# Optimization experiments

Hardware: AMD Instinct MI355X
Metric: run time of the kernel (lower is better)

## Reference

```python
import jax, jax.numpy as jnp
import numpy as np

N = 50000
E = 800000
IN_CH = 256
HID = 32
HEADS = 4
OUT_CH = 40
NEG_SLOPE = 0.2
BN_EPS = 1e-5


def _gat_conv(x, W, att_src, att_dst, bias, src, dst, num_nodes, concat):
    # x: [N, F_in]; W: [F_in, H*C]; att_src/att_dst: [H, C]
    H, C = att_src.shape
    h = (x @ W).reshape(num_nodes, H, C)            # [N, H, C]
    a_src = (h * att_src[None]).sum(-1)             # [N, H]
    a_dst = (h * att_dst[None]).sum(-1)             # [N, H]
    e = jax.nn.leaky_relu(a_src[src] + a_dst[dst], NEG_SLOPE)  # [Etot, H]
    # segment softmax over incoming edges of each destination node
    m = jax.ops.segment_max(e, dst, num_segments=num_nodes)    # [N, H]
    ex = jnp.exp(e - m[dst])
    s = jax.ops.segment_sum(ex, dst, num_segments=num_nodes)   # [N, H]
    alpha = ex / (s[dst] + 1e-16)                   # [Etot, H]
    out = jax.ops.segment_sum(h[src] * alpha[:, :, None], dst,
                              num_segments=num_nodes)          # [N, H, C]
    out = out.reshape(num_nodes, H * C) if concat else out.mean(axis=1)
    return out + bias


def setup_inputs() -> dict:
    key = jax.random.key(0)
    ks = jax.random.split(key, 12)
    x = jax.random.normal(ks[0], (N, IN_CH), dtype=jnp.float32)
    edge_index = jax.random.randint(ks[1], (2, E), 0, N, dtype=jnp.int64)
    # layer 1: in -> heads*hid, concat
    W1 = jax.random.normal(ks[2], (IN_CH, HEADS * HID), dtype=jnp.float32) * (1.0 / np.sqrt(IN_CH))
    att_src1 = jax.random.normal(ks[3], (HEADS, HID), dtype=jnp.float32) * 0.1
    att_dst1 = jax.random.normal(ks[4], (HEADS, HID), dtype=jnp.float32) * 0.1
    b1 = jnp.zeros((HEADS * HID,), dtype=jnp.float32)
    # batch norm over hidden*heads features
    gamma = jnp.ones((HEADS * HID,), dtype=jnp.float32)
    beta = jnp.zeros((HEADS * HID,), dtype=jnp.float32)
    # layer 2: heads*hid -> out, heads=1, mean (concat=False)
    W2 = jax.random.normal(ks[5], (HEADS * HID, OUT_CH), dtype=jnp.float32) * (1.0 / np.sqrt(HEADS * HID))
    att_src2 = jax.random.normal(ks[6], (1, OUT_CH), dtype=jnp.float32) * 0.1
    att_dst2 = jax.random.normal(ks[7], (1, OUT_CH), dtype=jnp.float32) * 0.1
    b2 = jnp.zeros((OUT_CH,), dtype=jnp.float32)
    return {"x": x, "edge_index": edge_index, "W1": W1, "att_src1": att_src1,
            "att_dst1": att_dst1, "b1": b1, "gamma": gamma, "beta": beta,
            "W2": W2, "att_src2": att_src2, "att_dst2": att_dst2, "b2": b2}


def reference(x, edge_index, W1, att_src1, att_dst1, b1, gamma, beta,
              W2, att_src2, att_dst2, b2):
    num_nodes = x.shape[0]
    loops = jnp.arange(num_nodes, dtype=edge_index.dtype)
    src = jnp.concatenate([edge_index[0], loops])   # add self-loops (PyG default)
    dst = jnp.concatenate([edge_index[1], loops])
    h = _gat_conv(x, W1, att_src1, att_dst1, b1, src, dst, num_nodes, concat=True)
    # BatchNorm over nodes (training-mode batch statistics)
    mu = h.mean(axis=0)
    var = h.var(axis=0)
    h = (h - mu) * jax.lax.rsqrt(var + BN_EPS) * gamma + beta
    h = jax.nn.elu(h)
    out = _gat_conv(h, W2, att_src2, att_dst2, b2, src, dst, num_nodes, concat=False)
    return out
```

## Files before the change

kernel.cpp:

```cpp
#include <hip/hip_runtime.h>

#define NN 50000
#define EE 800000
#define FIN 256
#define F1 128
#define F2 40
#define CAP 48
#define G1B ((NN + 127) / 128)
#define FILLB ((EE + 255) / 256)
#define PB ((NN + 63) / 64)

typedef unsigned int u32;
typedef unsigned short u16;

static __device__ __forceinline__ u32 f2bf(float f) {
  u32 u = __float_as_uint(f);
  return (u + 0x7FFFu + ((u >> 16) & 1u)) >> 16;
}
#define BF_LO(u) __uint_as_float((u) << 16)
#define BF_HI(u) __uint_as_float((u) & 0xFFFF0000u)

__global__ __launch_bounds__(256) void g1f_kernel(const float* __restrict__ x,
                                                  const float* __restrict__ W1,
                                                  const float* __restrict__ att_src,
                                                  const float* __restrict__ att_dst,
                                                  u32* __restrict__ h1bf,
                                                  float* __restrict__ a_src,
                                                  float* __restrict__ a_dst,
                                                  const int* __restrict__ ei,
                                                  int* __restrict__ cnt,
                                                  int* __restrict__ csr) {
  __shared__ float Alds[16 * 132];
  __shared__ float Blds[16 * 128];
  __shared__ float att_s[128], att_d[128];
  const int t = threadIdx.x;

  if (blockIdx.x >= G1B) {
    int e = (blockIdx.x - G1B) * 256 + t;
    if (e < EE) {
      int src = ei[e];
      int dst = ei[EE + e];
      int p = atomicAdd(cnt + dst, 1);
      if (p < CAP) csr[dst * CAP + p] = src;
    }
    return;
  }

  if (t < 128) { att_s[t] = att_src[t]; att_d[t] = att_dst[t]; }
  const int m0 = blockIdx.x * 128;
  const int arow = t >> 1;
  const int akk = (t & 1) * 8;
  const int brow = t >> 4;
  const int bc = (t & 15) * 8;
  const int ty = t >> 4;
  const int tx = t & 15;

  float acc[8][8];
#pragma unroll
  for (int i = 0; i < 8; ++i)
#pragma unroll
    for (int j = 0; j < 8; ++j) acc[i][j] = 0.f;

  for (int k0 = 0; k0 < FIN; k0 += 16) {
    float4 a0 = {0.f, 0.f, 0.f, 0.f}, a1 = {0.f, 0.f, 0.f, 0.f};
    int gr = m0 + arow;
    if (gr < NN) {
      a0 = *(const float4*)(x + (size_t)gr * FIN + k0 + akk);
      a1 = *(const float4*)(x + (size_t)gr * FIN + k0 + akk + 4);
    }
    float4 b0 = *(const float4*)(W1 + (size_t)(k0 + brow) * F1 + bc);
    float4 b1 = *(const float4*)(W1 + (size_t)(k0 + brow) * F1 + bc + 4);
    __syncthreads();
    Alds[(akk + 0) * 132 + arow] = a0.x;
    Alds[(akk + 1) * 132 + arow] = a0.y;
    Alds[(akk + 2) * 132 + arow] = a0.z;
    Alds[(akk + 3) * 132 + arow] = a0.w;
    Alds[(akk + 4) * 132 + arow] = a1.x;
    Alds[(akk + 5) * 132 + arow] = a1.y;
    Alds[(akk + 6) * 132 + arow] = a1.z;
    Alds[(akk + 7) * 132 + arow] = a1.w;
    *(float4*)(Blds + brow * 128 + bc) = b0;
    *(float4*)(Blds + brow * 128 + bc + 4) = b1;
    __syncthreads();
#pragma unroll
    for (int k = 0; k < 16; ++k) {
      float4 av0 = *(const float4*)(Alds + k * 132 + ty * 8);
      float4 av1 = *(const float4*)(Alds + k * 132 + ty * 8 + 4);
      float4 bv0 = *(const float4*)(Blds + k * 128 + tx * 8);
      float4 bv1 = *(const float4*)(Blds + k * 128 + tx * 8 + 4);
      float aa[8] = {av0.x, av0.y, av0.z, av0.w, av1.x, av1.y, av1.z, av1.w};
      float bb[8] = {bv0.x, bv0.y, bv0.z, bv0.w, bv1.x, bv1.y, bv1.z, bv1.w};
#pragma unroll
      for (int i = 0; i < 8; ++i)
#pragma unroll
        for (int j = 0; j < 8; ++j) acc[i][j] = fmaf(aa[i], bb[j], acc[i][j]);
    }
  }
#pragma unroll
  for (int i = 0; i < 8; ++i) {
    int gr = m0 + ty * 8 + i;
    if (gr < NN) {
      uint4 w;
      w.x = f2bf(acc[i][0]) | (f2bf(acc[i][1]) << 16);
      w.y = f2bf(acc[i][2]) | (f2bf(acc[i][3]) << 16);
      w.z = f2bf(acc[i][4]) | (f2bf(acc[i][5]) << 16);
      w.w = f2bf(acc[i][6]) | (f2bf(acc[i][7]) << 16);
      *(uint4*)(h1bf + ((size_t)(tx >> 2) * NN + gr) * 16 + (tx & 3) * 4) = w;
    }
  }
#pragma unroll
  for (int i = 0; i < 8; ++i) {
    float ps = 0.f, pd = 0.f;
#pragma unroll
    for (int j = 0; j < 8; ++j) {
      int c = tx * 8 + j;
      ps += acc[i][j] * att_s[c];
      pd += acc[i][j] * att_d[c];
    }
    ps += __shfl_xor(ps, 1); pd += __shfl_xor(pd, 1);
    ps += __shfl_xor(ps, 2); pd += __shfl_xor(pd, 2);
    if ((tx & 3) == 0) {
      int gr = m0 + ty * 8 + i;
      if (gr < NN) {
        int head = tx >> 2;
        a_src[gr * 4 + head] = ps;
        a_dst[gr * 4 + head] = pd;
      }
    }
  }
}

__global__ __launch_bounds__(256) void gather1_kernel(const int* __restrict__ cnt,
                                                      const int* __restrict__ csr,
                                                      const float* __restrict__ a_src,
                                                      const float* __restrict__ a_dst,
                                                      const u32* __restrict__ h1bf,
                                                      const float* __restrict__ b1,
                                                      float* __restrict__ h1b,
                                                      float* __restrict__ bnsum,
                                                      float* __restrict__ bnsq) {
  __shared__ float bns[32], bnq[32];
  int t = threadIdx.x;
  if (t < 32) { bns[t] = 0.f; bnq[t] = 0.f; }
  __syncthreads();
  int d = blockIdx.x;
  int xcd = d & 7;
  int p = xcd >> 1;
  int nb = ((d >> 3) << 1) + (xcd & 1);
  int n = nb * 64 + (t >> 2);
  int l = t & 3;
  int f0 = p * 32 + l * 8;
  if (n < NN) {
    float adst = a_dst[n * 4 + p];
    float acc[8] = {0.f, 0.f, 0.f, 0.f, 0.f, 0.f, 0.f, 0.f};
    float ssum = 0.f;
    const u32* hb = h1bf + (size_t)p * NN * 16 + l * 4;
    {
      float e0 = a_src[n * 4 + p] + adst;
      e0 = e0 > 0.f ? e0 : 0.2f * e0;
      float x0 = __expf(e0);
      uint4 q = *(const uint4*)(hb + (size_t)n * 16);
      acc[0] = fmaf(x0, BF_LO(q.x), acc[0]); acc[1] = fmaf(x0, BF_HI(q.x), acc[1]);
      acc[2] = fmaf(x0, BF_LO(q.y), acc[2]); acc[3] = fmaf(x0, BF_HI(q.y), acc[3]);
      acc[4] = fmaf(x0, BF_LO(q.z), acc[4]); acc[5] = fmaf(x0, BF_HI(q.z), acc[5]);
      acc[6] = fmaf(x0, BF_LO(q.w), acc[6]); acc[7] = fmaf(x0, BF_HI(q.w), acc[7]);
      ssum += x0;
    }
    const int* row = csr + n * CAP;
    int m = cnt[n]; if (m > CAP) m = CAP;
    int i = 0;
    for (; i + 3 < m; i += 4) {
      int4 s4 = *(const int4*)(row + i);
      float e0 = a_src[s4.x * 4 + p] + adst;
      float e1 = a_src[s4.y * 4 + p] + adst;
      float e2 = a_src[s4.z * 4 + p] + adst;
      float e3 = a_src[s4.w * 4 + p] + adst;
      uint4 q0 = *(const uint4*)(hb + (size_t)s4.x * 16);
      uint4 q1 = *(const uint4*)(hb + (size_t)s4.y * 16);
      uint4 q2 = *(const uint4*)(hb + (size_t)s4.z * 16);
      uint4 q3 = *(const uint4*)(hb + (size_t)s4.w * 16);
      e0 = e0 > 0.f ? e0 : 0.2f * e0;  float x0 = __expf(e0);
      e1 = e1 > 0.f ? e1 : 0.2f * e1;  float x1 = __expf(e1);
      e2 = e2 > 0.f ? e2 : 0.2f * e2;  float x2 = __expf(e2);
      e3 = e3 > 0.f ? e3 : 0.2f * e3;  float x3 = __expf(e3);
      acc[0] = fmaf(x0, BF_LO(q0.x), acc[0]); acc[1] = fmaf(x0, BF_HI(q0.x), acc[1]);
      acc[2] = fmaf(x0, BF_LO(q0.y), acc[2]); acc[3] = fmaf(x0, BF_HI(q0.y), acc[3]);
      acc[4] = fmaf(x0, BF_LO(q0.z), acc[4]); acc[5] = fmaf(x0, BF_HI(q0.z), acc[5]);
      acc[6] = fmaf(x0, BF_LO(q0.w), acc[6]); acc[7] = fmaf(x0, BF_HI(q0.w), acc[7]);
      acc[0] = fmaf(x1, BF_LO(q1.x), acc[0]); acc[1] = fmaf(x1, BF_HI(q1.x), acc[1]);
      acc[2] = fmaf(x1, BF_LO(q1.y), acc[2]); acc[3] = fmaf(x1, BF_HI(q1.y), acc[3]);
      acc[4] = fmaf(x1, BF_LO(q1.z), acc[4]); acc[5] = fmaf(x1, BF_HI(q1.z), acc[5]);
      acc[6] = fmaf(x1, BF_LO(q1.w), acc[6]); acc[7] = fmaf(x1, BF_HI(q1.w), acc[7]);
      acc[0] = fmaf(x2, BF_LO(q2.x), acc[0]); acc[1] = fmaf(x2, BF_HI(q2.x), acc[1]);
      acc[2] = fmaf(x2, BF_LO(q2.y), acc[2]); acc[3] = fmaf(x2, BF_HI(q2.y), acc[3]);
      acc[4] = fmaf(x2, BF_LO(q2.z), acc[4]); acc[5] = fmaf(x2, BF_HI(q2.z), acc[5]);
      acc[6] = fmaf(x2, BF_LO(q2.w), acc[6]); acc[7] = fmaf(x2, BF_HI(q2.w), acc[7]);
      acc[0] = fmaf(x3, BF_LO(q3.x), acc[0]); acc[1] = fmaf(x3, BF_HI(q3.x), acc[1]);
      acc[2] = fmaf(x3, BF_LO(q3.y), acc[2]); acc[3] = fmaf(x3, BF_HI(q3.y), acc[3]);
      acc[4] = fmaf(x3, BF_LO(q3.z), acc[4]); acc[5] = fmaf(x3, BF_HI(q3.z), acc[5]);
      acc[6] = fmaf(x3, BF_LO(q3.w), acc[6]); acc[7] = fmaf(x3, BF_HI(q3.w), acc[7]);
      ssum += x0 + x1 + x2 + x3;
    }
    for (; i < m; ++i) {
      int s0 = row[i];
      float e0 = a_src[s0 * 4 + p] + adst;
      e0 = e0 > 0.f ? e0 : 0.2f * e0;
      float x0 = __expf(e0);
      uint4 q = *(const uint4*)(hb + (size_t)s0 * 16);
      acc[0] = fmaf(x0, BF_LO(q.x), acc[0]); acc[1] = fmaf(x0, BF_HI(q.x), acc[1]);
      acc[2] = fmaf(x0, BF_LO(q.y), acc[2]); acc[3] = fmaf(x0, BF_HI(q.y), acc[3]);
      acc[4] = fmaf(x0, BF_LO(q.z), acc[4]); acc[5] = fmaf(x0, BF_HI(q.z), acc[5]);
      acc[6] = fmaf(x0, BF_LO(q.w), acc[6]); acc[7] = fmaf(x0, BF_HI(q.w), acc[7]);
      ssum += x0;
    }
    float inv = 1.f / (ssum + 1e-16f);
    float4 b0 = *(const float4*)(b1 + f0);
    float4 b4 = *(const float4*)(b1 + f0 + 4);
    float o[8];
    o[0] = acc[0] * inv + b0.x; o[1] = acc[1] * inv + b0.y;
    o[2] = acc[2] * inv + b0.z; o[3] = acc[3] * inv + b0.w;
    o[4] = acc[4] * inv + b4.x; o[5] = acc[5] * inv + b4.y;
    o[6] = acc[6] * inv + b4.z; o[7] = acc[7] * inv + b4.w;
    float4 w0 = {o[0], o[1], o[2], o[3]};
    float4 w1 = {o[4], o[5], o[6], o[7]};
    *(float4*)(h1b + (size_t)n * F1 + f0) = w0;
    *(float4*)(h1b + (size_t)n * F1 + f0 + 4) = w1;
    int lb = l * 8;
#pragma unroll
    for (int j = 0; j < 8; ++j) {
      atomicAdd(&bns[lb + j], o[j]);
      atomicAdd(&bnq[lb + j], o[j] * o[j]);
    }
  }
  __syncthreads();
  if (t < 32) {
    atomicAdd(bnsum + p * 32 + t, bns[t]);
    atomicAdd(bnsq + p * 32 + t, bnq[t]);
  }
}

__global__ __launch_bounds__(256) void gemm2_kernel(const float* __restrict__ hpre,
                                                    const float* __restrict__ W2,
                                                    const float* __restrict__ bnsum,
                                                    const float* __restrict__ bnsq,
                                                    const float* __restrict__ gamma,
                                                    const float* __restrict__ beta,
                                                    u16* __restrict__ h2a,
                                                    u16* __restrict__ h2b,
                                                    const float* __restrict__ att_src2,
                                                    const float* __restrict__ att_dst2,
                                                    float* __restrict__ a_src2,
                                                    float* __restrict__ a_dst2) {
  __shared__ float Wlds[128 * 40];
  __shared__ float Alds[16 * 128];
  __shared__ float sc[128], sh[128];
  int t = threadIdx.x;
  for (int i = t; i < 128 * 40; i += 256) Wlds[i] = W2[i];
  if (t < 128) {
    const float invN = 1.f / (float)NN;
    float mu = bnsum[t] * invN;
    float var = bnsq[t] * invN - mu * mu;
    float s = gamma[t] * rsqrtf(var + 1e-5f);
    sc[t] = s;
    sh[t] = beta[t] - mu * s;
  }
  int tr = t >> 3;
  int tc = t & 7;
  float as5[5], ad5[5];
#pragma unroll
  for (int j = 0; j < 5; ++j) { as5[j] = att_src2[tc * 5 + j]; ad5[j] = att_dst2[tc * 5 + j]; }
  int n0 = blockIdx.x * 128;
  int lrow = t >> 1;
  int lkk = (t & 1) * 8;
  float acc[4][5];
#pragma unroll
  for (int i = 0; i < 4; ++i)
#pragma unroll
    for (int j = 0; j < 5; ++j) acc[i][j] = 0.f;

  for (int k0 = 0; k0 < F1; k0 += 16) {
    float av[8];
    int gn = n0 + lrow;
    if (gn < NN) {
      float4 v0 = *(const float4*)(hpre + (size_t)gn * F1 + k0 + lkk);
      float4 v1 = *(const float4*)(hpre + (size_t)gn * F1 + k0 + lkk + 4);
      av[0] = v0.x; av[1] = v0.y; av[2] = v0.z; av[3] = v0.w;
      av[4] = v1.x; av[5] = v1.y; av[6] = v1.z; av[7] = v1.w;
    } else {
#pragma unroll
      for (int j = 0; j < 8; ++j) av[j] = 0.f;
    }
    __syncthreads();
#pragma unroll
    for (int j = 0; j < 8; ++j) {
      int kg = k0 + lkk + j;
      float a = av[j] * sc[kg] + sh[kg];
      a = a > 0.f ? a : (__expf(a) - 1.f);
      Alds[(lkk + j) * 128 + lrow] = a;
    }
    __syncthreads();
#pragma unroll
    for (int k = 0; k < 16; ++k) {
      float4 a4 = *(const float4*)(Alds + k * 128 + tr * 4);
      float aa[4] = {a4.x, a4.y, a4.z, a4.w};
      float w[5];
#pragma unroll
      for (int j = 0; j < 5; ++j) w[j] = Wlds[(k0 + k) * 40 + tc * 5 + j];
#pragma unroll
      for (int i = 0; i < 4; ++i)
#pragma unroll
        for (int j = 0; j < 5; ++j) acc[i][j] = fmaf(aa[i], w[j], acc[i][j]);
    }
  }
#pragma unroll
  for (int i = 0; i < 4; ++i) {
    int gn = n0 + tr * 4 + i;
    if (gn < NN) {
#pragma unroll
      for (int j = 0; j < 5; ++j) {
        int f = tc * 5 + j;
        u16 v = (u16)f2bf(acc[i][j]);
        if (f < 32) h2a[(size_t)gn * 32 + f] = v;
        else        h2b[(size_t)gn * 8 + (f - 32)] = v;
      }
    }
  }
#pragma unroll
  for (int i = 0; i < 4; ++i) {
    float ps = 0.f, pd = 0.f;
#pragma unroll
    for (int j = 0; j < 5; ++j) { ps += acc[i][j] * as5[j]; pd += acc[i][j] * ad5[j]; }
#pragma unroll
    for (int off = 1; off < 8; off <<= 1) {
      ps += __shfl_xor(ps, off);
      pd += __shfl_xor(pd, off);
    }
    if (tc == 0) {
      int gn = n0 + tr * 4 + i;
      if (gn < NN) { a_src2[gn] = ps; a_dst2[gn] = pd; }
    }
  }
}

__global__ __launch_bounds__(256) void gather2_kernel(const int* __restrict__ cnt,
                                                      const int* __restrict__ csr,
                                                      const float* __restrict__ a_src,
                                                      const float* __restrict__ a_dst,
                                                      const u32* __restrict__ h2a,
                                                      const u32* __restrict__ h2b,
                                                      const float* __restrict__ b2,
                                                      float* __restrict__ out) {
  int t = threadIdx.x;
  int n = blockIdx.x * 32 + (t >> 3);
  if (n >= NN) return;
  int l = t & 7;
  bool act = (l < 5);
  bool isA = (l < 4);
  float adst = a_dst[n];
  float acc[8] = {0.f, 0.f, 0.f, 0.f, 0.f, 0.f, 0.f, 0.f};
  float ssum = 0.f;
  const uint4 zz = {0u, 0u, 0u, 0u};
  {
    float e0 = a_src[n] + adst;
    e0 = e0 > 0.f ? e0 : 0.2f * e0;
    float x0 = __expf(e0);
    uint4 q = act ? (isA ? *(const uint4*)(h2a + (size_t)n * 16 + l * 4)
                         : *(const uint4*)(h2b + (size_t)n * 4)) : zz;
    acc[0] = fmaf(x0, BF_LO(q.x), acc[0]); acc[1] = fmaf(x0, BF_HI(q.x), acc[1]);
    acc[2] = fmaf(x0, BF_LO(q.y), acc[2]); acc[3] = fmaf(x0, BF_HI(q.y), acc[3]);
    acc[4] = fmaf(x0, BF_LO(q.z), acc[4]); acc[5] = fmaf(x0, BF_HI(q.z), acc[5]);
    acc[6] = fmaf(x0, BF_LO(q.w), acc[6]); acc[7] = fmaf(x0, BF_HI(q.w), acc[7]);
    ssum += x0;
  }
  const int* row = csr + n * CAP;
  int m = cnt[n]; if (m > CAP) m = CAP;
  int i = 0;
  for (; i + 3 < m; i += 4) {
    int4 s4 = *(const int4*)(row + i);
    float e0 = a_src[s4.x] + adst;
    float e1 = a_src[s4.y] + adst;
    float e2 = a_src[s4.z] + adst;
    float e3 = a_src[s4.w] + adst;
    uint4 q0 = act ? (isA ? *(const uint4*)(h2a + (size_t)s4.x * 16 + l * 4)
                          : *(const uint4*)(h2b + (size_t)s4.x * 4)) : zz;
    uint4 q1 = act ? (isA ? *(const uint4*)(h2a + (size_t)s4.y * 16 + l * 4)
                          : *(const uint4*)(h2b + (size_t)s4.y * 4)) : zz;
    uint4 q2 = act ? (isA ? *(const uint4*)(h2a + (size_t)s4.z * 16 + l * 4)
                          : *(const uint4*)(h2b + (size_t)s4.z * 4)) : zz;
    uint4 q3 = act ? (isA ? *(const uint4*)(h2a + (size_t)s4.w * 16 + l * 4)
                          : *(const uint4*)(h2b + (size_t)s4.w * 4)) : zz;
    e0 = e0 > 0.f ? e0 : 0.2f * e0;  float x0 = __expf(e0);
    e1 = e1 > 0.f ? e1 : 0.2f * e1;  float x1 = __expf(e1);
    e2 = e2 > 0.f ? e2 : 0.2f * e2;  float x2 = __expf(e2);
    e3 = e3 > 0.f ? e3 : 0.2f * e3;  float x3 = __expf(e3);
    acc[0] = fmaf(x0, BF_LO(q0.x), acc[0]); acc[1] = fmaf(x0, BF_HI(q0.x), acc[1]);
    acc[2] = fmaf(x0, BF_LO(q0.y), acc[2]); acc[3] = fmaf(x0, BF_HI(q0.y), acc[3]);
    acc[4] = fmaf(x0, BF_LO(q0.z), acc[4]); acc[5] = fmaf(x0, BF_HI(q0.z), acc[5]);
    acc[6] = fmaf(x0, BF_LO(q0.w), acc[6]); acc[7] = fmaf(x0, BF_HI(q0.w), acc[7]);
    acc[0] = fmaf(x1, BF_LO(q1.x), acc[0]); acc[1] = fmaf(x1, BF_HI(q1.x), acc[1]);
    acc[2] = fmaf(x1, BF_LO(q1.y), acc[2]); acc[3] = fmaf(x1, BF_HI(q1.y), acc[3]);
    acc[4] = fmaf(x1, BF_LO(q1.z), acc[4]); acc[5] = fmaf(x1, BF_HI(q1.z), acc[5]);
    acc[6] = fmaf(x1, BF_LO(q1.w), acc[6]); acc[7] = fmaf(x1, BF_HI(q1.w), acc[7]);
    acc[0] = fmaf(x2, BF_LO(q2.x), acc[0]); acc[1] = fmaf(x2, BF_HI(q2.x), acc[1]);
    acc[2] = fmaf(x2, BF_LO(q2.y), acc[2]); acc[3] = fmaf(x2, BF_HI(q2.y), acc[3]);
    acc[4] = fmaf(x2, BF_LO(q2.z), acc[4]); acc[5] = fmaf(x2, BF_HI(q2.z), acc[5]);
    acc[6] = fmaf(x2, BF_LO(q2.w), acc[6]); acc[7] = fmaf(x2, BF_HI(q2.w), acc[7]);
    acc[0] = fmaf(x3, BF_LO(q3.x), acc[0]); acc[1] = fmaf(x3, BF_HI(q3.x), acc[1]);
    acc[2] = fmaf(x3, BF_LO(q3.y), acc[2]); acc[3] = fmaf(x3, BF_HI(q3.y), acc[3]);
    acc[4] = fmaf(x3, BF_LO(q3.z), acc[4]); acc[5] = fmaf(x3, BF_HI(q3.z), acc[5]);
    acc[6] = fmaf(x3, BF_LO(q3.w), acc[6]); acc[7] = fmaf(x3, BF_HI(q3.w), acc[7]);
    ssum += x0 + x1 + x2 + x3;
  }
  for (; i < m; ++i) {
    int s0 = row[i];
    float e0 = a_src[s0] + adst;
    e0 = e0 > 0.f ? e0 : 0.2f * e0;
    float x0 = __expf(e0);
    uint4 q = act ? (isA ? *(const uint4*)(h2a + (size_t)s0 * 16 + l * 4)
                         : *(const uint4*)(h2b + (size_t)s0 * 4)) : zz;
    acc[0] = fmaf(x0, BF_LO(q.x), acc[0]); acc[1] = fmaf(x0, BF_HI(q.x), acc[1]);
    acc[2] = fmaf(x0, BF_LO(q.y), acc[2]); acc[3] = fmaf(x0, BF_HI(q.y), acc[3]);
    acc[4] = fmaf(x0, BF_LO(q.z), acc[4]); acc[5] = fmaf(x0, BF_HI(q.z), acc[5]);
    acc[6] = fmaf(x0, BF_LO(q.w), acc[6]); acc[7] = fmaf(x0, BF_HI(q.w), acc[7]);
    ssum += x0;
  }
  float inv = 1.f / (ssum + 1e-16f);
  if (act) {
    float* op = out + (size_t)n * F2 + l * 8;
#pragma unroll
    for (int j = 0; j < 8; ++j) op[j] = acc[j] * inv + b2[l * 8 + j];
  }
}

extern "C" void kernel_launch(void* const* d_in, const int* in_sizes, int n_in,
                              void* d_out, int out_size, void* d_ws, size_t ws_size,
                              hipStream_t stream) {
  const float* x        = (const float*)d_in[0];
  const int*   ei       = (const int*)d_in[1];
  const float* W1       = (const float*)d_in[2];
  const float* att_src1 = (const float*)d_in[3];
  const float* att_dst1 = (const float*)d_in[4];
  const float* b1       = (const float*)d_in[5];
  const float* gamma    = (const float*)d_in[6];
  const float* beta     = (const float*)d_in[7];
  const float* W2       = (const float*)d_in[8];
  const float* att_src2 = (const float*)d_in[9];
  const float* att_dst2 = (const float*)d_in[10];
  const float* b2       = (const float*)d_in[11];
  float* out = (float*)d_out;

  int* cnt      = (int*)d_ws;
  float* bnsum  = (float*)(cnt + 50048);
  float* bnsq   = bnsum + 128;
  int* csr      = (int*)(bnsq + 128);
  u32* h1bf     = (u32*)(csr + NN * CAP);
  float* h1b    = (float*)(h1bf + 3200000);
  u32* h2a      = (u32*)(h1b + 6400000);
  u32* h2b      = h2a + 800000;
  float* a_src1 = (float*)(h2b + 200000);
  float* a_dst1 = a_src1 + 200000;
  float* a_src2 = a_dst1 + 200000;
  float* a_dst2 = a_src2 + 50000;

  hipMemsetAsync(cnt, 0, (50048 + 256) * sizeof(int), stream);

  g1f_kernel<<<G1B + FILLB, 256, 0, stream>>>(x, W1, att_src1, att_dst1,
                                              h1bf, a_src1, a_dst1,
                                              ei, cnt, csr);
  gather1_kernel<<<4 * PB, 256, 0, stream>>>(cnt, csr, a_src1, a_dst1,
                                             h1bf, b1, h1b, bnsum, bnsq);
  gemm2_kernel<<<(NN + 127) / 128, 256, 0, stream>>>(h1b, W2, bnsum, bnsq,
                                                     gamma, beta,
                                                     (u16*)h2a, (u16*)h2b,
                                                     att_src2, att_dst2,
                                                     a_src2, a_dst2);
  gather2_kernel<<<(NN + 31) / 32, 256, 0, stream>>>(cnt, csr, a_src2, a_dst2,
                                                     h2a, h2b, b2, out);
}
```

Before: 318.5 us.

## Split each node's edge list across more lanes in both gather kernels

```diff
diff --git a/kernel.cpp b/kernel.cpp
--- a/kernel.cpp
+++ b/kernel.cpp
@@ -8,7 +8,8 @@
 #define CAP 48
 #define G1B ((NN + 127) / 128)
 #define FILLB ((EE + 255) / 256)
-#define PB ((NN + 63) / 64)
+#define G1PB 3126
+#define G2B ((NN + 15) / 16)
 
 typedef unsigned int u32;
 typedef unsigned short u16;
@@ -147,15 +148,17 @@
   int xcd = d & 7;
   int p = xcd >> 1;
   int nb = ((d >> 3) << 1) + (xcd & 1);
-  int n = nb * 64 + (t >> 2);
-  int l = t & 3;
+  int n = nb * 16 + (t >> 4);
+  int sub = t & 15;
+  int g = sub >> 2;
+  int l = sub & 3;
   int f0 = p * 32 + l * 8;
+  float acc[8] = {0.f, 0.f, 0.f, 0.f, 0.f, 0.f, 0.f, 0.f};
+  float ssum = 0.f;
   if (n < NN) {
     float adst = a_dst[n * 4 + p];
-    float acc[8] = {0.f, 0.f, 0.f, 0.f, 0.f, 0.f, 0.f, 0.f};
-    float ssum = 0.f;
     const u32* hb = h1bf + (size_t)p * NN * 16 + l * 4;
-    {
+    if (g == 0) {
       float e0 = a_src[n * 4 + p] + adst;
       e0 = e0 > 0.f ? e0 : 0.2f * e0;
       float x0 = __expf(e0);
@@ -168,21 +171,16 @@
     }
     const int* row = csr + n * CAP;
     int m = cnt[n]; if (m > CAP) m = CAP;
-    int i = 0;
-    for (; i + 3 < m; i += 4) {
-      int4 s4 = *(const int4*)(row + i);
-      float e0 = a_src[s4.x * 4 + p] + adst;
-      float e1 = a_src[s4.y * 4 + p] + adst;
-      float e2 = a_src[s4.z * 4 + p] + adst;
-      float e3 = a_src[s4.w * 4 + p] + adst;
-      uint4 q0 = *(const uint4*)(hb + (size_t)s4.x * 16);
-      uint4 q1 = *(const uint4*)(hb + (size_t)s4.y * 16);
-      uint4 q2 = *(const uint4*)(hb + (size_t)s4.z * 16);
-      uint4 q3 = *(const uint4*)(hb + (size_t)s4.w * 16);
+    int i = g;
+    for (; i + 4 < m; i += 8) {
+      int s0 = row[i];
+      int s1 = row[i + 4];
+      float e0 = a_src[s0 * 4 + p] + adst;
+      float e1 = a_src[s1 * 4 + p] + adst;
+      uint4 q0 = *(const uint4*)(hb + (size_t)s0 * 16);
+      uint4 q1 = *(const uint4*)(hb + (size_t)s1 * 16);
       e0 = e0 > 0.f ? e0 : 0.2f * e0;  float x0 = __expf(e0);
       e1 = e1 > 0.f ? e1 : 0.2f * e1;  float x1 = __expf(e1);
-      e2 = e2 > 0.f ? e2 : 0.2f * e2;  float x2 = __expf(e2);
-      e3 = e3 > 0.f ? e3 : 0.2f * e3;  float x3 = __expf(e3);
       acc[0] = fmaf(x0, BF_LO(q0.x), acc[0]); acc[1] = fmaf(x0, BF_HI(q0.x), acc[1]);
       acc[2] = fmaf(x0, BF_LO(q0.y), acc[2]); acc[3] = fmaf(x0, BF_HI(q0.y), acc[3]);
       acc[4] = fmaf(x0, BF_LO(q0.z), acc[4]); acc[5] = fmaf(x0, BF_HI(q0.z), acc[5]);
@@ -191,17 +189,9 @@
       acc[2] = fmaf(x1, BF_LO(q1.y), acc[2]); acc[3] = fmaf(x1, BF_HI(q1.y), acc[3]);
       acc[4] = fmaf(x1, BF_LO(q1.z), acc[4]); acc[5] = fmaf(x1, BF_HI(q1.z), acc[5]);
       acc[6] = fmaf(x1, BF_LO(q1.w), acc[6]); acc[7] = fmaf(x1, BF_HI(q1.w), acc[7]);
-      acc[0] = fmaf(x2, BF_LO(q2.x), acc[0]); acc[1] = fmaf(x2, BF_HI(q2.x), acc[1]);
-      acc[2] = fmaf(x2, BF_LO(q2.y), acc[2]); acc[3] = fmaf(x2, BF_HI(q2.y), acc[3]);
-      acc[4] = fmaf(x2, BF_LO(q2.z), acc[4]); acc[5] = fmaf(x2, BF_HI(q2.z), acc[5]);
-      acc[6] = fmaf(x2, BF_LO(q2.w), acc[6]); acc[7] = fmaf(x2, BF_HI(q2.w), acc[7]);
-      acc[0] = fmaf(x3, BF_LO(q3.x), acc[0]); acc[1] = fmaf(x3, BF_HI(q3.x), acc[1]);
-      acc[2] = fmaf(x3, BF_LO(q3.y), acc[2]); acc[3] = fmaf(x3, BF_HI(q3.y), acc[3]);
-      acc[4] = fmaf(x3, BF_LO(q3.z), acc[4]); acc[5] = fmaf(x3, BF_HI(q3.z), acc[5]);
-      acc[6] = fmaf(x3, BF_LO(q3.w), acc[6]); acc[7] = fmaf(x3, BF_HI(q3.w), acc[7]);
-      ssum += x0 + x1 + x2 + x3;
-    }
-    for (; i < m; ++i) {
+      ssum += x0 + x1;
+    }
+    for (; i < m; i += 4) {
       int s0 = row[i];
       float e0 = a_src[s0 * 4 + p] + adst;
       e0 = e0 > 0.f ? e0 : 0.2f * e0;
@@ -213,6 +203,15 @@
       acc[6] = fmaf(x0, BF_LO(q.w), acc[6]); acc[7] = fmaf(x0, BF_HI(q.w), acc[7]);
       ssum += x0;
     }
+  }
+#pragma unroll
+  for (int j = 0; j < 8; ++j) {
+    acc[j] += __shfl_xor(acc[j], 4);
+    acc[j] += __shfl_xor(acc[j], 8);
+  }
+  ssum += __shfl_xor(ssum, 4);
+  ssum += __shfl_xor(ssum, 8);
+  if (n < NN && g == 0) {
     float inv = 1.f / (ssum + 1e-16f);
     float4 b0 = *(const float4*)(b1 + f0);
     float4 b4 = *(const float4*)(b1 + f0 + 4);
@@ -351,16 +350,17 @@
                                                       const float* __restrict__ b2,
                                                       float* __restrict__ out) {
   int t = threadIdx.x;
-  int n = blockIdx.x * 32 + (t >> 3);
+  int n = blockIdx.x * 16 + (t >> 4);
   if (n >= NN) return;
   int l = t & 7;
+  int g = (t >> 3) & 1;
   bool act = (l < 5);
   bool isA = (l < 4);
   float adst = a_dst[n];
   float acc[8] = {0.f, 0.f, 0.f, 0.f, 0.f, 0.f, 0.f, 0.f};
   float ssum = 0.f;
   const uint4 zz = {0u, 0u, 0u, 0u};
-  {
+  if (g == 0) {
     float e0 = a_src[n] + adst;
     e0 = e0 > 0.f ? e0 : 0.2f * e0;
     float x0 = __expf(e0);
@@ -374,58 +374,63 @@
   }
   const int* row = csr + n * CAP;
   int m = cnt[n]; if (m > CAP) m = CAP;
-  int i = 0;
-  for (; i + 3 < m; i += 4) {
-    int4 s4 = *(const int4*)(row + i);
-    float e0 = a_src[s4.x] + adst;
-    float e1 = a_src[s4.y] + adst;
-    float e2 = a_src[s4.z] + adst;
-    float e3 = a_src[s4.w] + adst;
-    uint4 q0 = act ? (isA ? *(const uint4*)(h2a + (size_t)s4.x * 16 + l * 4)
-                          : *(const uint4*)(h2b + (size_t)s4.x * 4)) : zz;
-    uint4 q1 = act ? (isA ? *(const uint4*)(h2a + (size_t)s4.y * 16 + l * 4)
-                          : *(const uint4*)(h2b + (size_t)s4.y * 4)) : zz;
-    uint4 q2 = act ? (isA ? *(const uint4*)(h2a + (size_t)s4.z * 16 + l * 4)
-                          : *(const uint4*)(h2b + (size_t)s4.z * 4)) : zz;
-    uint4 q3 = act ? (isA ? *(const uint4*)(h2a + (size_t)s4.w * 16 + l * 4)
-                          : *(const uint4*)(h2b + (size_t)s4.w * 4)) : zz;
-    e0 = e0 > 0.f ? e0 : 0.2f * e0;  float x0 = __expf(e0);
-    e1 = e1 > 0.f ? e1 : 0.2f * e1;  float x1 = __expf(e1);
-    e2 = e2 > 0.f ? e2 : 0.2f * e2;  float x2 = __expf(e2);
-    e3 = e3 > 0.f ? e3 : 0.2f * e3;  float x3 = __expf(e3);
-    acc[0] = fmaf(x0, BF_LO(q0.x), acc[0]); acc[1] = fmaf(x0, BF_HI(q0.x), acc[1]);
-    acc[2] = fmaf(x0, BF_LO(q0.y), acc[2]); acc[3] = fmaf(x0, BF_HI(q0.y), acc[3]);
-    acc[4] = fmaf(x0, BF_LO(q0.z), acc[4]); acc[5] = fmaf(x0, BF_HI(q0.z), acc[5]);
-    acc[6] = fmaf(x0, BF_LO(q0.w), acc[6]); acc[7] = fmaf(x0, BF_HI(q0.w), acc[7]);
-    acc[0] = fmaf(x1, BF_LO(q1.x), acc[0]); acc[1] = fmaf(x1, BF_HI(q1.x), acc[1]);
-    acc[2] = fmaf(x1, BF_LO(q1.y), acc[2]); acc[3] = fmaf(x1, BF_HI(q1.y), acc[3]);
-    acc[4] = fmaf(x1, BF_LO(q1.z), acc[4]); acc[5] = fmaf(x1, BF_HI(q1.z), acc[5]);
-    acc[6] = fmaf(x1, BF_LO(q1.w), acc[6]); acc[7] = fmaf(x1, BF_HI(q1.w), acc[7]);
-    acc[0] = fmaf(x2, BF_LO(q2.x), acc[0]); acc[1] = fmaf(x2, BF_HI(q2.x), acc[1]);
-    acc[2] = fmaf(x2, BF_LO(q2.y), acc[2]); acc[3] = fmaf(x2, BF_HI(q2.y), acc[3]);
-    acc[4] = fmaf(x2, BF_LO(q2.z), acc[4]); acc[5] = fmaf(x2, BF_HI(q2.z), acc[5]);
-    acc[6] = fmaf(x2, BF_LO(q2.w), acc[6]); acc[7] = fmaf(x2, BF_HI(q2.w), acc[7]);
-    acc[0] = fmaf(x3, BF_LO(q3.x), acc[0]); acc[1] = fmaf(x3, BF_HI(q3.x), acc[1]);
-    acc[2] = fmaf(x3, BF_LO(q3.y), acc[2]); acc[3] = fmaf(x3, BF_HI(q3.y), acc[3]);
-    acc[4] = fmaf(x3, BF_LO(q3.z), acc[4]); acc[5] = fmaf(x3, BF_HI(q3.z), acc[5]);
-    acc[6] = fmaf(x3, BF_LO(q3.w), acc[6]); acc[7] = fmaf(x3, BF_HI(q3.w), acc[7]);
-    ssum += x0 + x1 + x2 + x3;
-  }
-  for (; i < m; ++i) {
-    int s0 = row[i];
-    float e0 = a_src[s0] + adst;
-    e0 = e0 > 0.f ? e0 : 0.2f * e0;
-    float x0 = __expf(e0);
-    uint4 q = act ? (isA ? *(const uint4*)(h2a + (size_t)s0 * 16 + l * 4)
-                         : *(const uint4*)(h2b + (size_t)s0 * 4)) : zz;
-    acc[0] = fmaf(x0, BF_LO(q.x), acc[0]); acc[1] = fmaf(x0, BF_HI(q.x), acc[1]);
-    acc[2] = fmaf(x0, BF_LO(q.y), acc[2]); acc[3] = fmaf(x0, BF_HI(q.y), acc[3]);
-    acc[4] = fmaf(x0, BF_LO(q.z), acc[4]); acc[5] = fmaf(x0, BF_HI(q.z), acc[5]);
-    acc[6] = fmaf(x0, BF_LO(q.w), acc[6]); acc[7] = fmaf(x0, BF_HI(q.w), acc[7]);
-    ssum += x0;
-  }
+  for (int c = 4 * g; c < m; c += 8) {
+    if (c + 4 <= m) {
+      int4 s4 = *(const int4*)(row + c);
+      float e0 = a_src[s4.x] + adst;
+      float e1 = a_src[s4.y] + adst;
+      float e2 = a_src[s4.z] + adst;
+      float e3 = a_src[s4.w] + adst;
+      uint4 q0 = act ? (isA ? *(const uint4*)(h2a + (size_t)s4.x * 16 + l * 4)
+                            : *(const uint4*)(h2b + (size_t)s4.x * 4)) : zz;
+      uint4 q1 = act ? (isA ? *(const uint4*)(h2a + (size_t)s4.y * 16 + l * 4)
+                            : *(const uint4*)(h2b + (size_t)s4.y * 4)) : zz;
+      uint4 q2 = act ? (isA ? *(const uint4*)(h2a + (size_t)s4.z * 16 + l * 4)
+                            : *(const uint4*)(h2b + (size_t)s4.z * 4)) : zz;
+      uint4 q3 = act ? (isA ? *(const uint4*)(h2a + (size_t)s4.w * 16 + l * 4)
+                            : *(const uint4*)(h2b + (size_t)s4.w * 4)) : zz;
+      e0 = e0 > 0.f ? e0 : 0.2f * e0;  float x0 = __expf(e0);
+      e1 = e1 > 0.f ? e1 : 0.2f * e1;  float x1 = __expf(e1);
+      e2 = e2 > 0.f ? e2 : 0.2f * e2;  float x2 = __expf(e2);
+      e3 = e3 > 0.f ? e3 : 0.2f * e3;  float x3 = __expf(e3);
+      acc[0] = fmaf(x0, BF_LO(q0.x), acc[0]); acc[1] = fmaf(x0, BF_HI(q0.x), acc[1]);
+      acc[2] = fmaf(x0, BF_LO(q0.y), acc[2]); acc[3] = fmaf(x0, BF_HI(q0.y), acc[3]);
+      acc[4] = fmaf(x0, BF_LO(q0.z), acc[4]); acc[5] = fmaf(x0, BF_HI(q0.z), acc[5]);
+      acc[6] = fmaf(x0, BF_LO(q0.w), acc[6]); acc[7] = fmaf(x0, BF_HI(q0.w), acc[7]);
+      acc[0] = fmaf(x1, BF_LO(q1.x), acc[0]); acc[1] = fmaf(x1, BF_HI(q1.x), acc[1]);
+      acc[2] = fmaf(x1, BF_LO(q1.y), acc[2]); acc[3] = fmaf(x1, BF_HI(q1.y), acc[3]);
+      acc[4] = fmaf(x1, BF_LO(q1.z), acc[4]); acc[5] = fmaf(x1, BF_HI(q1.z), acc[5]);
+      acc[6] = fmaf(x1, BF_LO(q1.w), acc[6]); acc[7] = fmaf(x1, BF_HI(q1.w), acc[7]);
+      acc[0] = fmaf(x2, BF_LO(q2.x), acc[0]); acc[1] = fmaf(x2, BF_HI(q2.x), acc[1]);
+      acc[2] = fmaf(x2, BF_LO(q2.y), acc[2]); acc[3] = fmaf(x2, BF_HI(q2.y), acc[3]);
+      acc[4] = fmaf(x2, BF_LO(q2.z), acc[4]); acc[5] = fmaf(x2, BF_HI(q2.z), acc[5]);
+      acc[6] = fmaf(x2, BF_LO(q2.w), acc[6]); acc[7] = fmaf(x2, BF_HI(q2.w), acc[7]);
+      acc[0] = fmaf(x3, BF_LO(q3.x), acc[0]); acc[1] = fmaf(x3, BF_HI(q3.x), acc[1]);
+      acc[2] = fmaf(x3, BF_LO(q3.y), acc[2]); acc[3] = fmaf(x3, BF_HI(q3.y), acc[3]);
+      acc[4] = fmaf(x3, BF_LO(q3.z), acc[4]); acc[5] = fmaf(x3, BF_HI(q3.z), acc[5]);
+      acc[6] = fmaf(x3, BF_LO(q3.w), acc[6]); acc[7] = fmaf(x3, BF_HI(q3.w), acc[7]);
+      ssum += x0 + x1 + x2 + x3;
+    } else {
+      for (int i = c; i < m; ++i) {
+        int s0 = row[i];
+        float e0 = a_src[s0] + adst;
+        e0 = e0 > 0.f ? e0 : 0.2f * e0;
+        float x0 = __expf(e0);
+        uint4 q = act ? (isA ? *(const uint4*)(h2a + (size_t)s0 * 16 + l * 4)
+                             : *(const uint4*)(h2b + (size_t)s0 * 4)) : zz;
+        acc[0] = fmaf(x0, BF_LO(q.x), acc[0]); acc[1] = fmaf(x0, BF_HI(q.x), acc[1]);
+        acc[2] = fmaf(x0, BF_LO(q.y), acc[2]); acc[3] = fmaf(x0, BF_HI(q.y), acc[3]);
+        acc[4] = fmaf(x0, BF_LO(q.z), acc[4]); acc[5] = fmaf(x0, BF_HI(q.z), acc[5]);
+        acc[6] = fmaf(x0, BF_LO(q.w), acc[6]); acc[7] = fmaf(x0, BF_HI(q.w), acc[7]);
+        ssum += x0;
+      }
+    }
+  }
+#pragma unroll
+  for (int j = 0; j < 8; ++j) acc[j] += __shfl_xor(acc[j], 8);
+  ssum += __shfl_xor(ssum, 8);
   float inv = 1.f / (ssum + 1e-16f);
-  if (act) {
+  if (g == 0 && act) {
     float* op = out + (size_t)n * F2 + l * 8;
 #pragma unroll
     for (int j = 0; j < 8; ++j) op[j] = acc[j] * inv + b2[l * 8 + j];
@@ -467,13 +472,13 @@
   g1f_kernel<<<G1B + FILLB, 256, 0, stream>>>(x, W1, att_src1, att_dst1,
                                               h1bf, a_src1, a_dst1,
                                               ei, cnt, csr);
-  gather1_kernel<<<4 * PB, 256, 0, stream>>>(cnt, csr, a_src1, a_dst1,
-                                             h1bf, b1, h1b, bnsum, bnsq);
+  gather1_kernel<<<(G1PB / 2) * 8, 256, 0, stream>>>(cnt, csr, a_src1, a_dst1,
+                                                     h1bf, b1, h1b, bnsum, bnsq);
   gemm2_kernel<<<(NN + 127) / 128, 256, 0, stream>>>(h1b, W2, bnsum, bnsq,
                                                      gamma, beta,
                                                      (u16*)h2a, (u16*)h2b,
                                                      att_src2, att_dst2,
                                                      a_src2, a_dst2);
-  gather2_kernel<<<(NN + 31) / 32, 256, 0, stream>>>(cnt, csr, a_src2, a_dst2,
-                                                     h2a, h2b, b2, out);
-}
+  gather2_kernel<<<G2B, 256, 0, stream>>>(cnt, csr, a_src2, a_dst2,
+                                          h2a, h2b, b2, out);
+}
```

Result: no change. 313.1 us (-1.7%).
